# Kernel tuning notes

Hardware: AMD Instinct MI355X
Metric: run time of the kernel (lower is better)

The kernel has to match this reference:

```python
import jax, jax.numpy as jnp
import numpy as np

HIDDEN = 3072
INTER = 8192
B, S = 4, 2048


def setup_inputs() -> dict:
    key = jax.random.key(0)
    k1, k2, k3, k4, k5 = jax.random.split(key, 5)
    hidden_states = jax.random.normal(k1, (B, S, HIDDEN), dtype=jnp.float32)
    # int8-valued quantized weights (stored as int32), per-output-channel scales
    gate_up_w_q = jax.random.randint(k2, (2 * INTER, HIDDEN), -128, 128, dtype=jnp.int32)
    gate_up_scale = jax.random.uniform(k3, (2 * INTER,), dtype=jnp.float32) * 0.01
    down_w_q = jax.random.randint(k4, (HIDDEN, INTER), -128, 128, dtype=jnp.int32)
    down_scale = jax.random.uniform(k5, (HIDDEN,), dtype=jnp.float32) * 0.01
    return {
        "hidden_states": hidden_states,
        "gate_up_w_q": gate_up_w_q,
        "gate_up_scale": gate_up_scale,
        "down_w_q": down_w_q,
        "down_scale": down_scale,
    }


def reference(hidden_states, gate_up_w_q, gate_up_scale, down_w_q, down_scale):
    # Inline dequant: W = W_q * scale (per output channel)
    w_gu = gate_up_w_q.astype(jnp.float32) * gate_up_scale[:, None]   # [2I, H]
    up_states = jnp.einsum("bsh,oh->bso", hidden_states, w_gu)        # [B, S, 2I]
    gate, up = jnp.split(up_states, 2, axis=-1)                       # each [B, S, I]
    h = up * jax.nn.silu(gate)                                        # SwiGLU
    w_d = down_w_q.astype(jnp.float32) * down_scale[:, None]          # [H, I]
    return jnp.einsum("bsi,hi->bsh", h, w_d)                          # [B, S, H]
```

## Files before the change

### kernel.cpp

```cpp
#include <hip/hip_runtime.h>
#include <hip/hip_bf16.h>

#define HIDDEN 3072
#define INTER  8192
#define NTOK   8192

typedef __attribute__((ext_vector_type(8))) short bf16x8;
typedef __attribute__((ext_vector_type(4))) float f32x4;

__device__ __forceinline__ void gload_lds16(const void* g, void* l) {
  __builtin_amdgcn_global_load_lds(
      (const __attribute__((address_space(1))) void*)g,
      (__attribute__((address_space(3))) void*)l, 16, 0, 0);
}

__device__ __forceinline__ unsigned short f2bf(float f) {
  unsigned int u = __builtin_bit_cast(unsigned int, f);
  u += 0x7fffu + ((u >> 16) & 1u);
  return (unsigned short)(u >> 16);
}


__global__ void cvt_f32_bf16(const float* __restrict__ in,
                             unsigned short* __restrict__ out, int n4) {
  int i = blockIdx.x * blockDim.x + threadIdx.x;
  if (i >= n4) return;
  float4 v = reinterpret_cast<const float4*>(in)[i];
  ushort4 o;
  o.x = f2bf(v.x); o.y = f2bf(v.y); o.z = f2bf(v.z); o.w = f2bf(v.w);
  reinterpret_cast<ushort4*>(out)[i] = o;
}

__global__ void cvt_i32_bf16(const int* __restrict__ in,
                             unsigned short* __restrict__ out, int n4) {
  int i = blockIdx.x * blockDim.x + threadIdx.x;
  if (i >= n4) return;
  int4 v = reinterpret_cast<const int4*>(in)[i];
  ushort4 o;
  o.x = f2bf((float)v.x); o.y = f2bf((float)v.y);
  o.z = f2bf((float)v.z); o.w = f2bf((float)v.w);
  reinterpret_cast<ushort4*>(out)[i] = o;
}

__global__ void cvt_wgu_perm(const int* __restrict__ in,
                             unsigned short* __restrict__ out) {
  int i4 = blockIdx.x * blockDim.x + threadIdx.x;
  const int RW = HIDDEN / 4;
  if (i4 >= 2 * INTER * RW) return;
  int rowp = i4 / RW;
  int col4 = i4 - rowp * RW;
  int c = ((rowp >> 5) << 4) + (rowp & 15);
  int u = (rowp >> 4) & 1;
  int srow = u * INTER + c;
  int4 v = reinterpret_cast<const int4*>(in)[(size_t)srow * RW + col4];
  ushort4 o;
  o.x = f2bf((float)v.x); o.y = f2bf((float)v.y);
  o.z = f2bf((float)v.z); o.w = f2bf((float)v.w);
  reinterpret_cast<ushort4*>(out)[i4] = o;
}


template<int K, int N, bool SWIGLU>
__global__ __launch_bounds__(512, 2) void gemm8p(
    const unsigned short* __restrict__ A,
    const unsigned short* __restrict__ B,
    const float* __restrict__ scale,
    void* __restrict__ outv)
{
  constexpr int NT = K / 64;
  __shared__ __align__(16) unsigned short lds[2][2][2][256 * 32];

  const int nbn = N / 256;
  const int nwg = (NTOK / 256) * nbn;
  int bid = blockIdx.x;
  int wg = (bid & 7) * (nwg >> 3) + (bid >> 3);
  const int bm = (wg / nbn) * 256;
  const int bn = (wg % nbn) * 256;

  const int tid  = threadIdx.x;
  const int lane = tid & 63;
  const int wid  = tid >> 6;
  const int wr = wid >> 2;
  const int wc = wid & 3;

  const int srow0 = tid >> 2;
  const int srow1 = 128 + (tid >> 2);
  const int scb   = tid & 3;

  const unsigned short* Ab = A + (size_t)bm * K;
  const unsigned short* Bb = B + (size_t)bn * K;

  auto stage = [&](const unsigned short* Gb, int op, int tt, int kh) {
    if (tt >= NT) return;
    int p = tt & 1;
    int kc = tt * 64 + kh * 32;
    unsigned short* lbase = &lds[p][op][kh][0];
    gload_lds16(Gb + (size_t)srow0 * K + kc + ((scb ^ (srow0 & 3)) * 8),
                lbase + (size_t)tid * 8);
    gload_lds16(Gb + (size_t)srow1 * K + kc + ((scb ^ (srow1 & 3)) * 8),
                lbase + (size_t)(512 + tid) * 8);
  };

  auto readA = [&](int p, int kh, int m) -> bf16x8 {
    int row = wr * 128 + m * 16 + (lane & 15);
    int cb = (lane >> 4) ^ (row & 3);
    return *(const bf16x8*)&lds[p][0][kh][row * 32 + cb * 8];
  };
  auto readB = [&](int p, int kh, int n) -> bf16x8 {
    int row = wc * 64 + n * 16 + (lane & 15);
    int cb = (lane >> 4) ^ (row & 3);
    return *(const bf16x8*)&lds[p][1][kh][row * 32 + cb * 8];
  };

  f32x4 acc[8][4] = {};
  bf16x8 af[8];

  stage(Ab, 0, 0, 0);
  stage(Bb, 1, 0, 0);
  stage(Ab, 0, 0, 1);
  stage(Bb, 1, 0, 1);
  asm volatile("s_waitcnt vmcnt(4)" ::: "memory");
  __builtin_amdgcn_s_barrier();

  for (int t = 0; t < NT; ++t) {
    const int pr = t & 1;
#pragma unroll
    for (int m = 0; m < 8; ++m) af[m] = readA(pr, 0, m);
    bf16x8 b0 = readB(pr, 0, 0);
    bf16x8 b1 = readB(pr, 0, 1);
    stage(Ab, 0, t + 1, 0);
    __builtin_amdgcn_s_barrier();
    __builtin_amdgcn_s_setprio(1);
#pragma unroll
    for (int m = 0; m < 8; ++m) {
      acc[m][0] = __builtin_amdgcn_mfma_f32_16x16x32_bf16(af[m], b0, acc[m][0], 0, 0, 0);
      acc[m][1] = __builtin_amdgcn_mfma_f32_16x16x32_bf16(af[m], b1, acc[m][1], 0, 0, 0);
    }
    __builtin_amdgcn_s_setprio(0);
    __builtin_amdgcn_s_barrier();

    b0 = readB(pr, 0, 2);
    b1 = readB(pr, 0, 3);
    stage(Bb, 1, t + 1, 0);
    __builtin_amdgcn_s_barrier();
    __builtin_amdgcn_s_setprio(1);
#pragma unroll
    for (int m = 0; m < 8; ++m) {
      acc[m][2] = __builtin_amdgcn_mfma_f32_16x16x32_bf16(af[m], b0, acc[m][2], 0, 0, 0);
      acc[m][3] = __builtin_amdgcn_mfma_f32_16x16x32_bf16(af[m], b1, acc[m][3], 0, 0, 0);
    }
    __builtin_amdgcn_s_setprio(0);
    if (t + 1 < NT) {
      asm volatile("s_waitcnt vmcnt(4)" ::: "memory");
    } else {
      asm volatile("s_waitcnt vmcnt(0)" ::: "memory");
    }
    __builtin_amdgcn_s_barrier();

#pragma unroll
    for (int m = 0; m < 8; ++m) af[m] = readA(pr, 1, m);
    b0 = readB(pr, 1, 0);
    b1 = readB(pr, 1, 1);
    stage(Ab, 0, t + 1, 1);
    __builtin_amdgcn_s_barrier();
    __builtin_amdgcn_s_setprio(1);
#pragma unroll
    for (int m = 0; m < 8; ++m) {
      acc[m][0] = __builtin_amdgcn_mfma_f32_16x16x32_bf16(af[m], b0, acc[m][0], 0, 0, 0);
      acc[m][1] = __builtin_amdgcn_mfma_f32_16x16x32_bf16(af[m], b1, acc[m][1], 0, 0, 0);
    }
    __builtin_amdgcn_s_setprio(0);
    __builtin_amdgcn_s_barrier();

    b0 = readB(pr, 1, 2);
    b1 = readB(pr, 1, 3);
    stage(Bb, 1, t + 1, 1);
    __builtin_amdgcn_s_barrier();
    __builtin_amdgcn_s_setprio(1);
#pragma unroll
    for (int m = 0; m < 8; ++m) {
      acc[m][2] = __builtin_amdgcn_mfma_f32_16x16x32_bf16(af[m], b0, acc[m][2], 0, 0, 0);
      acc[m][3] = __builtin_amdgcn_mfma_f32_16x16x32_bf16(af[m], b1, acc[m][3], 0, 0, 0);
    }
    __builtin_amdgcn_s_setprio(0);
    asm volatile("s_waitcnt vmcnt(4)" ::: "memory");
    __builtin_amdgcn_s_barrier();
  }

  const int crow0 = (lane >> 4) * 4;
  const int ccol  = lane & 15;
  if constexpr (SWIGLU) {
    unsigned short* H = (unsigned short*)outv;
    const int hbase = (bn >> 1) + wc * 32;
#pragma unroll
    for (int np = 0; np < 2; ++np) {
      int hcol = hbase + np * 16 + ccol;
      float sg = scale[hcol];
      float su = scale[INTER + hcol];
#pragma unroll
      for (int m = 0; m < 8; ++m) {
#pragma unroll
        for (int j = 0; j < 4; ++j) {
          int row = bm + wr * 128 + m * 16 + crow0 + j;
          float g = acc[m][2 * np + 0][j] * sg;
          float u = acc[m][2 * np + 1][j] * su;
          float s = g / (1.0f + __expf(-g));
          H[(size_t)row * INTER + hcol] = f2bf(u * s);
        }
      }
    }
  } else {
    float* O = (float*)outv;
#pragma unroll
    for (int n = 0; n < 4; ++n) {
      int col = bn + wc * 64 + n * 16 + ccol;
      float sc = scale[col];
#pragma unroll
      for (int m = 0; m < 8; ++m) {
#pragma unroll
        for (int j = 0; j < 4; ++j) {
          int row = bm + wr * 128 + m * 16 + crow0 + j;
          O[(size_t)row * N + col] = acc[m][n][j] * sc;
        }
      }
    }
  }
}


extern "C" void kernel_launch(void* const* d_in, const int* in_sizes, int n_in,
                              void* d_out, int out_size, void* d_ws, size_t ws_size,
                              hipStream_t stream) {
  (void)in_sizes; (void)n_in; (void)out_size; (void)ws_size;

  const float* hidden = (const float*)d_in[0];
  const int*   guq    = (const int*)d_in[1];
  const float* gus    = (const float*)d_in[2];
  const int*   dwq    = (const int*)d_in[3];
  const float* dsc    = (const float*)d_in[4];
  float* out = (float*)d_out;

  char* ws = (char*)d_ws;
  unsigned short* xb  = (unsigned short*)(ws);
  unsigned short* wgu = (unsigned short*)(ws + 50331648ull);
  unsigned short* wd  = (unsigned short*)(ws + 150994944ull);
  unsigned short* hb  = (unsigned short*)(ws + 201326592ull);

  {
    int n4 = NTOK * HIDDEN / 4;
    cvt_f32_bf16<<<(n4 + 255) / 256, 256, 0, stream>>>(hidden, xb, n4);
  }
  {
    int n4 = 2 * INTER * HIDDEN / 4;
    cvt_wgu_perm<<<(n4 + 255) / 256, 256, 0, stream>>>(guq, wgu);
  }
  {
    int n4 = HIDDEN * INTER / 4;
    cvt_i32_bf16<<<(n4 + 255) / 256, 256, 0, stream>>>(dwq, wd, n4);
  }

  gemm8p<HIDDEN, 2 * INTER, true>
      <<<(NTOK / 256) * (2 * INTER / 256), 512, 0, stream>>>(xb, wgu, gus, hb);
  gemm8p<INTER, HIDDEN, false>
      <<<(NTOK / 256) * (HIDDEN / 256), 512, 0, stream>>>(hb, wd, dsc, out);
}
```

Baseline: 1.304 ms.

## Split-K the down projection GEMM with atomic accumulation and change LDS swizzle

The down-projection GEMM is split into two K slices, doubling its workgroup count from 384 to 768 so more CUs are busy. Partial results are combined with float atomicAdd into an output zeroed by a new kernel. The LDS XOR swizzle is also changed to use row>>1 to alter the bank-conflict pattern. The cost is an extra zeroing pass over the output, atomic traffic on 100MB of output, and nondeterministic summation order.

```diff
diff --git a/kernel.cpp b/kernel.cpp
--- a/kernel.cpp
+++ b/kernel.cpp
@@ -59,23 +59,33 @@
   reinterpret_cast<ushort4*>(out)[i4] = o;
 }
 
-
-template<int K, int N, bool SWIGLU>
+__global__ void zero_out(float* __restrict__ out, int n4) {
+  int stride = gridDim.x * blockDim.x;
+  for (int i = blockIdx.x * blockDim.x + threadIdx.x; i < n4; i += stride)
+    reinterpret_cast<float4*>(out)[i] = make_float4(0.f, 0.f, 0.f, 0.f);
+}
+
+
+template<int STRIDE, int KLEN, int N, int KSPLIT, int MODE>
 __global__ __launch_bounds__(512, 2) void gemm8p(
     const unsigned short* __restrict__ A,
     const unsigned short* __restrict__ B,
     const float* __restrict__ scale,
     void* __restrict__ outv)
 {
-  constexpr int NT = K / 64;
+  constexpr int NT = KLEN / 64;
   __shared__ __align__(16) unsigned short lds[2][2][2][256 * 32];
 
   const int nbn = N / 256;
-  const int nwg = (NTOK / 256) * nbn;
+  const int ntmn = (NTOK / 256) * nbn;
+  const int nwg = ntmn * KSPLIT;
   int bid = blockIdx.x;
   int wg = (bid & 7) * (nwg >> 3) + (bid >> 3);
-  const int bm = (wg / nbn) * 256;
-  const int bn = (wg % nbn) * 256;
+  const int kslice = wg / ntmn;
+  const int local = wg - kslice * ntmn;
+  const int bm = (local / nbn) * 256;
+  const int bn = (local % nbn) * 256;
+  const int koff = kslice * KLEN;
 
   const int tid  = threadIdx.x;
   const int lane = tid & 63;
@@ -87,28 +97,28 @@
   const int srow1 = 128 + (tid >> 2);
   const int scb   = tid & 3;
 
-  const unsigned short* Ab = A + (size_t)bm * K;
-  const unsigned short* Bb = B + (size_t)bn * K;
+  const unsigned short* Ab = A + (size_t)bm * STRIDE + koff;
+  const unsigned short* Bb = B + (size_t)bn * STRIDE + koff;
 
   auto stage = [&](const unsigned short* Gb, int op, int tt, int kh) {
     if (tt >= NT) return;
     int p = tt & 1;
     int kc = tt * 64 + kh * 32;
     unsigned short* lbase = &lds[p][op][kh][0];
-    gload_lds16(Gb + (size_t)srow0 * K + kc + ((scb ^ (srow0 & 3)) * 8),
+    gload_lds16(Gb + (size_t)srow0 * STRIDE + kc + ((scb ^ ((srow0 >> 1) & 3)) * 8),
                 lbase + (size_t)tid * 8);
-    gload_lds16(Gb + (size_t)srow1 * K + kc + ((scb ^ (srow1 & 3)) * 8),
+    gload_lds16(Gb + (size_t)srow1 * STRIDE + kc + ((scb ^ ((srow1 >> 1) & 3)) * 8),
                 lbase + (size_t)(512 + tid) * 8);
   };
 
   auto readA = [&](int p, int kh, int m) -> bf16x8 {
     int row = wr * 128 + m * 16 + (lane & 15);
-    int cb = (lane >> 4) ^ (row & 3);
+    int cb = (lane >> 4) ^ ((row >> 1) & 3);
     return *(const bf16x8*)&lds[p][0][kh][row * 32 + cb * 8];
   };
   auto readB = [&](int p, int kh, int n) -> bf16x8 {
     int row = wc * 64 + n * 16 + (lane & 15);
-    int cb = (lane >> 4) ^ (row & 3);
+    int cb = (lane >> 4) ^ ((row >> 1) & 3);
     return *(const bf16x8*)&lds[p][1][kh][row * 32 + cb * 8];
   };
 
@@ -189,7 +199,7 @@
 
   const int crow0 = (lane >> 4) * 4;
   const int ccol  = lane & 15;
-  if constexpr (SWIGLU) {
+  if constexpr (MODE == 1) {
     unsigned short* H = (unsigned short*)outv;
     const int hbase = (bn >> 1) + wc * 32;
 #pragma unroll
@@ -220,7 +230,7 @@
 #pragma unroll
         for (int j = 0; j < 4; ++j) {
           int row = bm + wr * 128 + m * 16 + crow0 + j;
-          O[(size_t)row * N + col] = acc[m][n][j] * sc;
+          atomicAdd(&O[(size_t)row * N + col], acc[m][n][j] * sc);
         }
       }
     }
@@ -258,9 +268,10 @@
     int n4 = HIDDEN * INTER / 4;
     cvt_i32_bf16<<<(n4 + 255) / 256, 256, 0, stream>>>(dwq, wd, n4);
   }
-
-  gemm8p<HIDDEN, 2 * INTER, true>
+  zero_out<<<2048, 256, 0, stream>>>(out, NTOK * HIDDEN / 4);
+
+  gemm8p<HIDDEN, HIDDEN, 2 * INTER, 1, 1>
       <<<(NTOK / 256) * (2 * INTER / 256), 512, 0, stream>>>(xb, wgu, gus, hb);
-  gemm8p<INTER, HIDDEN, false>
-      <<<(NTOK / 256) * (HIDDEN / 256), 512, 0, stream>>>(hb, wd, dsc, out);
-}
+  gemm8p<INTER, INTER / 2, HIDDEN, 2, 2>
+      <<<(NTOK / 256) * (HIDDEN / 256) * 2, 512, 0, stream>>>(hb, wd, dsc, out);
+}
```

Result: no change. 1.318 ms (+1.1%).

## Drop intra-phase barriers, regroup MFMAs as 4x4 blocks, and change LDS swizzle

Applied to the files above, without the earlier changes.

Within each k-half, the main loop no longer puts barriers between the two MFMA sub-phases. It loads all four B fragments up front and issues MFMAs in two 4x4 blocks over A rows 0-3 and then 4-7. The barriers it drops were only ordering work inside a phase, since the prefetch writes target the other LDS buffer. The LDS XOR swizzle now keys on (row>>1)&3 instead of row&3, to cut ds_read_b128 bank conflicts on the 64-byte rows. The template flag also becomes an int mode. The risks are scheduling changes across waves that are no longer in lockstep, and higher VGPR pressure from holding more fragments at once.

```diff
diff --git a/kernel.cpp b/kernel.cpp
--- a/kernel.cpp
+++ b/kernel.cpp
@@ -60,7 +60,7 @@
 }
 
 
-template<int K, int N, bool SWIGLU>
+template<int K, int N, int MODE>
 __global__ __launch_bounds__(512, 2) void gemm8p(
     const unsigned short* __restrict__ A,
     const unsigned short* __restrict__ B,
@@ -95,25 +95,25 @@
     int p = tt & 1;
     int kc = tt * 64 + kh * 32;
     unsigned short* lbase = &lds[p][op][kh][0];
-    gload_lds16(Gb + (size_t)srow0 * K + kc + ((scb ^ (srow0 & 3)) * 8),
+    gload_lds16(Gb + (size_t)srow0 * K + kc + ((scb ^ ((srow0 >> 1) & 3)) * 8),
                 lbase + (size_t)tid * 8);
-    gload_lds16(Gb + (size_t)srow1 * K + kc + ((scb ^ (srow1 & 3)) * 8),
+    gload_lds16(Gb + (size_t)srow1 * K + kc + ((scb ^ ((srow1 >> 1) & 3)) * 8),
                 lbase + (size_t)(512 + tid) * 8);
   };
 
   auto readA = [&](int p, int kh, int m) -> bf16x8 {
     int row = wr * 128 + m * 16 + (lane & 15);
-    int cb = (lane >> 4) ^ (row & 3);
+    int cb = (lane >> 4) ^ ((row >> 1) & 3);
     return *(const bf16x8*)&lds[p][0][kh][row * 32 + cb * 8];
   };
   auto readB = [&](int p, int kh, int n) -> bf16x8 {
     int row = wc * 64 + n * 16 + (lane & 15);
-    int cb = (lane >> 4) ^ (row & 3);
+    int cb = (lane >> 4) ^ ((row >> 1) & 3);
     return *(const bf16x8*)&lds[p][1][kh][row * 32 + cb * 8];
   };
 
   f32x4 acc[8][4] = {};
-  bf16x8 af[8];
+  bf16x8 af[4], ag[4], b[4];
 
   stage(Ab, 0, 0, 0);
   stage(Bb, 1, 0, 0);
@@ -124,31 +124,29 @@
 
   for (int t = 0; t < NT; ++t) {
     const int pr = t & 1;
-#pragma unroll
-    for (int m = 0; m < 8; ++m) af[m] = readA(pr, 0, m);
-    bf16x8 b0 = readB(pr, 0, 0);
-    bf16x8 b1 = readB(pr, 0, 1);
+
+#pragma unroll
+    for (int m = 0; m < 4; ++m) af[m] = readA(pr, 0, m);
+#pragma unroll
+    for (int n = 0; n < 4; ++n) b[n] = readB(pr, 0, n);
     stage(Ab, 0, t + 1, 0);
-    __builtin_amdgcn_s_barrier();
-    __builtin_amdgcn_s_setprio(1);
-#pragma unroll
-    for (int m = 0; m < 8; ++m) {
-      acc[m][0] = __builtin_amdgcn_mfma_f32_16x16x32_bf16(af[m], b0, acc[m][0], 0, 0, 0);
-      acc[m][1] = __builtin_amdgcn_mfma_f32_16x16x32_bf16(af[m], b1, acc[m][1], 0, 0, 0);
-    }
-    __builtin_amdgcn_s_setprio(0);
-    __builtin_amdgcn_s_barrier();
-
-    b0 = readB(pr, 0, 2);
-    b1 = readB(pr, 0, 3);
+    __builtin_amdgcn_s_setprio(1);
+#pragma unroll
+    for (int m = 0; m < 4; ++m)
+#pragma unroll
+      for (int n = 0; n < 4; ++n)
+        acc[m][n] = __builtin_amdgcn_mfma_f32_16x16x32_bf16(af[m], b[n], acc[m][n], 0, 0, 0);
+    __builtin_amdgcn_s_setprio(0);
+
+#pragma unroll
+    for (int m = 0; m < 4; ++m) ag[m] = readA(pr, 0, m + 4);
     stage(Bb, 1, t + 1, 0);
-    __builtin_amdgcn_s_barrier();
-    __builtin_amdgcn_s_setprio(1);
-#pragma unroll
-    for (int m = 0; m < 8; ++m) {
-      acc[m][2] = __builtin_amdgcn_mfma_f32_16x16x32_bf16(af[m], b0, acc[m][2], 0, 0, 0);
-      acc[m][3] = __builtin_amdgcn_mfma_f32_16x16x32_bf16(af[m], b1, acc[m][3], 0, 0, 0);
-    }
+    __builtin_amdgcn_s_setprio(1);
+#pragma unroll
+    for (int m = 0; m < 4; ++m)
+#pragma unroll
+      for (int n = 0; n < 4; ++n)
+        acc[m + 4][n] = __builtin_amdgcn_mfma_f32_16x16x32_bf16(ag[m], b[n], acc[m + 4][n], 0, 0, 0);
     __builtin_amdgcn_s_setprio(0);
     if (t + 1 < NT) {
       asm volatile("s_waitcnt vmcnt(4)" ::: "memory");
@@ -158,30 +156,27 @@
     __builtin_amdgcn_s_barrier();
 
 #pragma unroll
-    for (int m = 0; m < 8; ++m) af[m] = readA(pr, 1, m);
-    b0 = readB(pr, 1, 0);
-    b1 = readB(pr, 1, 1);
+    for (int m = 0; m < 4; ++m) af[m] = readA(pr, 1, m);
+#pragma unroll
+    for (int n = 0; n < 4; ++n) b[n] = readB(pr, 1, n);
     stage(Ab, 0, t + 1, 1);
-    __builtin_amdgcn_s_barrier();
-    __builtin_amdgcn_s_setprio(1);
-#pragma unroll
-    for (int m = 0; m < 8; ++m) {
-      acc[m][0] = __builtin_amdgcn_mfma_f32_16x16x32_bf16(af[m], b0, acc[m][0], 0, 0, 0);
-      acc[m][1] = __builtin_amdgcn_mfma_f32_16x16x32_bf16(af[m], b1, acc[m][1], 0, 0, 0);
-    }
-    __builtin_amdgcn_s_setprio(0);
-    __builtin_amdgcn_s_barrier();
-
-    b0 = readB(pr, 1, 2);
-    b1 = readB(pr, 1, 3);
+    __builtin_amdgcn_s_setprio(1);
+#pragma unroll
+    for (int m = 0; m < 4; ++m)
+#pragma unroll
+      for (int n = 0; n < 4; ++n)
+        acc[m][n] = __builtin_amdgcn_mfma_f32_16x16x32_bf16(af[m], b[n], acc[m][n], 0, 0, 0);
+    __builtin_amdgcn_s_setprio(0);
+
+#pragma unroll
+    for (int m = 0; m < 4; ++m) ag[m] = readA(pr, 1, m + 4);
     stage(Bb, 1, t + 1, 1);
-    __builtin_amdgcn_s_barrier();
-    __builtin_amdgcn_s_setprio(1);
-#pragma unroll
-    for (int m = 0; m < 8; ++m) {
-      acc[m][2] = __builtin_amdgcn_mfma_f32_16x16x32_bf16(af[m], b0, acc[m][2], 0, 0, 0);
-      acc[m][3] = __builtin_amdgcn_mfma_f32_16x16x32_bf16(af[m], b1, acc[m][3], 0, 0, 0);
-    }
+    __builtin_amdgcn_s_setprio(1);
+#pragma unroll
+    for (int m = 0; m < 4; ++m)
+#pragma unroll
+      for (int n = 0; n < 4; ++n)
+        acc[m + 4][n] = __builtin_amdgcn_mfma_f32_16x16x32_bf16(ag[m], b[n], acc[m + 4][n], 0, 0, 0);
     __builtin_amdgcn_s_setprio(0);
     asm volatile("s_waitcnt vmcnt(4)" ::: "memory");
     __builtin_amdgcn_s_barrier();
@@ -189,7 +184,7 @@
 
   const int crow0 = (lane >> 4) * 4;
   const int ccol  = lane & 15;
-  if constexpr (SWIGLU) {
+  if constexpr (MODE == 1) {
     unsigned short* H = (unsigned short*)outv;
     const int hbase = (bn >> 1) + wc * 32;
 #pragma unroll
@@ -259,8 +254,8 @@
     cvt_i32_bf16<<<(n4 + 255) / 256, 256, 0, stream>>>(dwq, wd, n4);
   }
 
-  gemm8p<HIDDEN, 2 * INTER, true>
+  gemm8p<HIDDEN, 2 * INTER, 1>
       <<<(NTOK / 256) * (2 * INTER / 256), 512, 0, stream>>>(xb, wgu, gus, hb);
-  gemm8p<INTER, HIDDEN, false>
+  gemm8p<INTER, HIDDEN, 2>
       <<<(NTOK / 256) * (HIDDEN / 256), 512, 0, stream>>>(hb, wd, dsc, out);
 }
```

Result: faster. 1.253 ms (-3.9%).
